# Kernel tuning notes

Hardware: AMD Instinct MI355X
Metric: run time of the kernel (lower is better)

## Reference

```python
import jax, jax.numpy as jnp
import numpy as np
import math

B, H, S, D = 2, 16, 2048, 128

def setup_inputs() -> dict:
    key = jax.random.key(0)
    kq, kk, kv = jax.random.split(key, 3)
    return {
        "query": jax.random.normal(kq, (B, H, S, D), dtype=jnp.float32),
        "key": jax.random.normal(kk, (B, H, S, D), dtype=jnp.float32),
        "value": jax.random.normal(kv, (B, H, S, D), dtype=jnp.float32),
        "m": 0,  # falsy mask: original's masked_fill was non-in-place (no-op) anyway
    }

def reference(query, key, value, m):
    d = query.shape[-1]
    # scores: [B, H, S, S]
    scores = jnp.einsum("bhqd,bhkd->bhqk", query, key) / math.sqrt(d)
    # NOTE: original torch code's masked_fill is not in-place, so the mask
    # never affects scores; we faithfully skip it (m is falsy here regardless).
    p_attn = jax.nn.softmax(scores, axis=-1)
    p_val = jnp.einsum("bhqk,bhkd->bhqd", p_attn, value)
    return (p_val, p_attn)
```

## Files before the change

### kernel.cpp

```cpp
#include <hip/hip_runtime.h>
#include <hip/hip_bf16.h>
#include <math.h>

#define S_LEN 2048
#define DHEAD 128
#define NH    32
#define BM    128
#define KT    32
#define NKT   (S_LEN / KT)
#define SCALE 0.08838834764831845f
#define CMAX  16.0f

typedef __attribute__((ext_vector_type(4))) float f32x4;
typedef __attribute__((ext_vector_type(8))) _Float16 f16x8;
typedef __attribute__((ext_vector_type(4))) unsigned short u16x4;
typedef __attribute__((ext_vector_type(8))) unsigned short u16x8;

static __device__ __forceinline__ f16x8 as_h8(u16x8 x) {
  return __builtin_bit_cast(f16x8, x);
}
static __device__ __forceinline__ unsigned short h16(float x) {
  _Float16 h = (_Float16)x;
  return __builtin_bit_cast(unsigned short, h);
}

#define BAR()                                                   \
  do {                                                          \
    __builtin_amdgcn_sched_barrier(0);                          \
    asm volatile("s_waitcnt lgkmcnt(0)" ::: "memory");          \
    __builtin_amdgcn_s_barrier();                               \
    __builtin_amdgcn_sched_barrier(0);                          \
  } while (0)

__global__ __launch_bounds__(512, 4) void attn_kernel(
    const float* __restrict__ Qg, const float* __restrict__ Kg,
    const float* __restrict__ Vg, float* __restrict__ out) {
  __shared__ __align__(16) unsigned short khf[2][KT * DHEAD];
  __shared__ __align__(16) unsigned short vtr[2][DHEAD * KT];

  const int tid = threadIdx.x;
  const int w  = tid >> 6;
  const int l  = tid & 63;
  const int lr = l & 15;
  const int lg = l >> 4;

  const int d_  = blockIdx.x;
  const int xcd = d_ & 7;
  const int slot = d_ >> 3;
  const int bh = xcd + 8 * (slot >> 4);
  const int qb = slot & 15;

  const size_t head_off = (size_t)bh * S_LEN * DHEAD;
  const float* Qh = Qg + head_off;
  const float* Kh = Kg + head_off;
  const float* Vh = Vg + head_off;
  float* Ov = out + head_off;
  float* Pa = out + (size_t)NH * S_LEN * DHEAD + (size_t)bh * S_LEN * S_LEN;

  const int ki0 = tid, ki1 = 512 + tid;
  const int kkv0 = ki0 >> 5, kd40 = ki0 & 31;
  const int kkv1 = ki1 >> 5, kd41 = ki1 & 31;
  const int vkv0 = (ki0 >> 2) & 31, vd40 = (ki0 & 3) | ((ki0 >> 7) << 2);
  const int vkv1 = (ki1 >> 2) & 31, vd41 = (ki1 & 3) | ((ki1 >> 7) << 2);

  float4 kxr0, kxr1, vx0, vx1;

  auto load_k = [&](int t) {
    const float4* s = (const float4*)(Kh + (size_t)t * KT * DHEAD);
    kxr0 = s[ki0];
    kxr1 = s[ki1];
  };
  auto load_v = [&](int t) {
    const float4* s = (const float4*)(Vh + (size_t)t * KT * DHEAD);
    vx0 = s[vkv0 * 32 + vd40];
    vx1 = s[vkv1 * 32 + vd41];
  };
  auto wk1 = [&](unsigned short* dst, int kv, int d4, float4 v) {
    u16x4 hv;
    hv[0] = h16(v.x); hv[1] = h16(v.y); hv[2] = h16(v.z); hv[3] = h16(v.w);
    *(u16x4*)&dst[kv * 128 + (((d4 >> 1) ^ (kv & 7)) << 3) + ((d4 & 1) << 2)] = hv;
  };
  auto write_k = [&](int b) {
    wk1(khf[b], kkv0, kd40, kxr0);
    wk1(khf[b], kkv1, kd41, kxr1);
  };
  auto wv1 = [&](unsigned short* dst, int kv, int d4, float4 v) {
    float f[4] = {v.x, v.y, v.z, v.w};
#pragma unroll
    for (int j = 0; j < 4; ++j) {
      int d = d4 * 4 + j;
      dst[d * 32 + (kv ^ (((d >> 1) & 3) << 3))] = h16(f[j]);
    }
  };
  auto write_v = [&](int b) {
    wv1(vtr[b], vkv0, vd40, vx0);
    wv1(vtr[b], vkv1, vd41, vx1);
  };
  auto ldk = [&](int b, int row, int kc) -> f16x8 {
    const unsigned short* base = khf[b] + row * 128;
    return as_h8(*(const u16x8*)&base[(((kc * 4 + lg) ^ (row & 7)) << 3)]);
  };

  load_k(0);
  const int qrow = qb * BM + w * 16 + lr;
  const float* qptr = Qh + (size_t)qrow * DHEAD;
  f16x8 qh[4];
#pragma unroll
  for (int kc = 0; kc < 4; ++kc) {
    const float4* qp4 = (const float4*)(qptr + kc * 32 + lg * 8);
    float4 a = qp4[0], b = qp4[1];
    float xs[8] = {a.x, a.y, a.z, a.w, b.x, b.y, b.z, b.w};
#pragma unroll
    for (int i = 0; i < 8; ++i) qh[kc][i] = (_Float16)(xs[i] * SCALE);
  }

  const f32x4 zero4 = {0.f, 0.f, 0.f, 0.f};

  float esum = 0.f;
  for (int t = 0; t < NKT; ++t) {
    const int b = t & 1;
    write_k(b);
    BAR();
    if (t + 1 < NKT) {
      load_k(t + 1);
    } else {
      load_k(0);
      load_v(0);
    }

    f32x4 sacc0 = zero4, sacc1 = zero4;
    __builtin_amdgcn_s_setprio(1);
#pragma unroll
    for (int kc = 0; kc < 4; ++kc) {
      f16x8 ka = ldk(b, lr, kc);
      f16x8 kb = ldk(b, lr + 16, kc);
      sacc0 = __builtin_amdgcn_mfma_f32_16x16x32_f16(ka, qh[kc], sacc0, 0, 0, 0);
      sacc1 = __builtin_amdgcn_mfma_f32_16x16x32_f16(kb, qh[kc], sacc1, 0, 0, 0);
    }
    __builtin_amdgcn_s_setprio(0);
#pragma unroll
    for (int r = 0; r < 4; ++r)
      esum += __expf(sacc0[r] - CMAX) + __expf(sacc1[r] - CMAX);
  }
  esum += __shfl_xor(esum, 16);
  esum += __shfl_xor(esum, 32);
  const float off_ = CMAX + logf(esum);

  f32x4 oacc[8];
#pragma unroll
  for (int dt = 0; dt < 8; ++dt) oacc[dt] = zero4;

  float* Prow = Pa + (size_t)(qb * BM + w * 16 + lr) * S_LEN;

  for (int t = 0; t < NKT; ++t) {
    const int b = t & 1;
    write_k(b);
    write_v(b);
    BAR();
    if (t + 1 < NKT) {
      load_k(t + 1);
      load_v(t + 1);
    }

    f32x4 sacc0 = zero4, sacc1 = zero4;
    __builtin_amdgcn_s_setprio(1);
#pragma unroll
    for (int kc = 0; kc < 4; ++kc) {
      f16x8 ka = ldk(b, lr, kc);
      f16x8 kb = ldk(b, lr + 16, kc);
      sacc0 = __builtin_amdgcn_mfma_f32_16x16x32_f16(ka, qh[kc], sacc0, 0, 0, 0);
      sacc1 = __builtin_amdgcn_mfma_f32_16x16x32_f16(kb, qh[kc], sacc1, 0, 0, 0);
    }
    __builtin_amdgcn_s_setprio(0);

    f32x4 pv0, pv1;
#pragma unroll
    for (int r = 0; r < 4; ++r) {
      pv0[r] = __expf(sacc0[r] - off_);
      pv1[r] = __expf(sacc1[r] - off_);
    }
    *(f32x4*)&Prow[t * KT + lg * 4] = pv0;
    *(f32x4*)&Prow[t * KT + 16 + lg * 4] = pv1;

    u16x8 pf;
    {
      unsigned pk[4];
#pragma unroll
      for (int r = 0; r < 4; ++r)
        pk[r] = __builtin_bit_cast(unsigned,
                  __builtin_amdgcn_cvt_pkrtz(pv0[r], pv1[r]));
      const int la = ((lg & 1) * 2) * 16 + lr;
      const int lb = la + 16;
      const bool hi = (lg & 2) != 0;
#pragma unroll
      for (int r = 0; r < 4; ++r) {
        unsigned ta = (unsigned)__shfl((int)pk[r], la, 64);
        unsigned tb = (unsigned)__shfl((int)pk[r], lb, 64);
        pf[r]     = (unsigned short)(hi ? (ta >> 16) : (ta & 0xffffu));
        pf[r + 4] = (unsigned short)(hi ? (tb >> 16) : (tb & 0xffffu));
      }
    }

    __builtin_amdgcn_s_setprio(1);
#pragma unroll
    for (int dt = 0; dt < 8; ++dt) {
      const int row = dt * 16 + lr;
      const unsigned short* vsrc = vtr[b];
      u16x8 vf = *(const u16x8*)&vsrc[row * 32 +
                                      ((lg * 8) ^ (((row >> 1) & 3) << 3))];
      oacc[dt] = __builtin_amdgcn_mfma_f32_16x16x32_f16(
          as_h8(pf), as_h8(vf), oacc[dt], 0, 0, 0);
    }
    __builtin_amdgcn_s_setprio(0);
  }

#pragma unroll
  for (int dt = 0; dt < 8; ++dt) {
#pragma unroll
    for (int r = 0; r < 4; ++r) {
      const int qloc = w * 16 + lg * 4 + r;
      Ov[(size_t)(qb * BM + qloc) * DHEAD + dt * 16 + lr] = oacc[dt][r];
    }
  }
}

extern "C" void kernel_launch(void* const* d_in, const int* in_sizes, int n_in,
                              void* d_out, int out_size, void* d_ws,
                              size_t ws_size, hipStream_t stream) {
  const float* Q = (const float*)d_in[0];
  const float* K = (const float*)d_in[1];
  const float* V = (const float*)d_in[2];
  float* out = (float*)d_out;
  (void)in_sizes; (void)n_in; (void)out_size; (void)d_ws; (void)ws_size;
  dim3 grid(NH * (S_LEN / BM));
  attn_kernel<<<grid, 512, 0, stream>>>(Q, K, V, out);
}
```

Before: 301.1 us.

## Shrink tiles to 64-row blocks with 16-key steps and 16x16x16 PV MFMA

Halves the query block to 64 rows and 256 threads, and halves the key tile to 16. The PV product now uses the 16x16x16 f16 MFMA directly on the score fragment, which removes the cross-lane shuffle repacking of probabilities. The V tile is stored transposed with a padded stride instead of an XOR swizzle. This trades less per-block K/V reuse and twice as many loop iterations and barriers for more blocks, simpler fragment handling and possibly better occupancy.

Result: slower. 438.2 us (+45.5%).

```diff
diff --git a/kernel.cpp b/kernel.cpp
--- a/kernel.cpp
+++ b/kernel.cpp
@@ -5,19 +5,24 @@
 #define S_LEN 2048
 #define DHEAD 128
 #define NH    32
-#define BM    128
-#define KT    32
+#define BM    64
+#define KT    16
 #define NKT   (S_LEN / KT)
+#define VPAD  20
 #define SCALE 0.08838834764831845f
 #define CMAX  16.0f
 
 typedef __attribute__((ext_vector_type(4))) float f32x4;
+typedef __attribute__((ext_vector_type(4))) _Float16 f16x4;
 typedef __attribute__((ext_vector_type(8))) _Float16 f16x8;
 typedef __attribute__((ext_vector_type(4))) unsigned short u16x4;
 typedef __attribute__((ext_vector_type(8))) unsigned short u16x8;
 
 static __device__ __forceinline__ f16x8 as_h8(u16x8 x) {
   return __builtin_bit_cast(f16x8, x);
+}
+static __device__ __forceinline__ f16x4 as_h4(u16x4 x) {
+  return __builtin_bit_cast(f16x4, x);
 }
 static __device__ __forceinline__ unsigned short h16(float x) {
   _Float16 h = (_Float16)x;
@@ -32,11 +37,11 @@
     __builtin_amdgcn_sched_barrier(0);                          \
   } while (0)
 
-__global__ __launch_bounds__(512, 4) void attn_kernel(
+__global__ __launch_bounds__(256) void attn_kernel(
     const float* __restrict__ Qg, const float* __restrict__ Kg,
     const float* __restrict__ Vg, float* __restrict__ out) {
   __shared__ __align__(16) unsigned short khf[2][KT * DHEAD];
-  __shared__ __align__(16) unsigned short vtr[2][DHEAD * KT];
+  __shared__ __align__(16) unsigned short vtr[2][DHEAD * VPAD];
 
   const int tid = threadIdx.x;
   const int w  = tid >> 6;
@@ -46,9 +51,9 @@
 
   const int d_  = blockIdx.x;
   const int xcd = d_ & 7;
-  const int slot = d_ >> 3;
-  const int bh = xcd + 8 * (slot >> 4);
-  const int qb = slot & 15;
+  const int idx = d_ >> 3;
+  const int bh = xcd + 8 * (idx >> 5);
+  const int qb = idx & 31;
 
   const size_t head_off = (size_t)bh * S_LEN * DHEAD;
   const float* Qh = Qg + head_off;
@@ -57,48 +62,45 @@
   float* Ov = out + head_off;
   float* Pa = out + (size_t)NH * S_LEN * DHEAD + (size_t)bh * S_LEN * S_LEN;
 
-  const int ki0 = tid, ki1 = 512 + tid;
-  const int kkv0 = ki0 >> 5, kd40 = ki0 & 31;
-  const int kkv1 = ki1 >> 5, kd41 = ki1 & 31;
-  const int vkv0 = (ki0 >> 2) & 31, vd40 = (ki0 & 3) | ((ki0 >> 7) << 2);
-  const int vkv1 = (ki1 >> 2) & 31, vd41 = (ki1 & 3) | ((ki1 >> 7) << 2);
-
-  float4 kxr0, kxr1, vx0, vx1;
-
+  const int kkv0 = tid >> 5, kd4 = tid & 31;
+  const int kkv1 = kkv0 + 8;
+  const int kaddr0 = kkv0 * 128 + (((kd4 >> 1) ^ (kkv0 & 7)) << 3) + ((kd4 & 1) << 2);
+  const int kaddr1 = kkv1 * 128 + (((kd4 >> 1) ^ (kkv1 & 7)) << 3) + ((kd4 & 1) << 2);
+  float4 kx0, kx1;
   auto load_k = [&](int t) {
     const float4* s = (const float4*)(Kh + (size_t)t * KT * DHEAD);
-    kxr0 = s[ki0];
-    kxr1 = s[ki1];
-  };
+    kx0 = s[tid];
+    kx1 = s[256 + tid];
+  };
+  auto write_k = [&](int b) {
+    u16x4 a, c;
+    a[0] = h16(kx0.x); a[1] = h16(kx0.y); a[2] = h16(kx0.z); a[3] = h16(kx0.w);
+    c[0] = h16(kx1.x); c[1] = h16(kx1.y); c[2] = h16(kx1.z); c[3] = h16(kx1.w);
+    *(u16x4*)&khf[b][kaddr0] = a;
+    *(u16x4*)&khf[b][kaddr1] = c;
+  };
+  auto ldk = [&](int b, int kc) -> f16x8 {
+    return as_h8(*(const u16x8*)&khf[b][lr * 128 + (((kc * 4 + lg) ^ (lr & 7)) << 3)]);
+  };
+
+  const int vkv = (tid >> 2) & 15;
+  const int vd40 = (tid & 3) | ((tid >> 6) << 2);
+  const int vd41 = vd40 + 16;
+  float4 vx0, vx1;
   auto load_v = [&](int t) {
     const float4* s = (const float4*)(Vh + (size_t)t * KT * DHEAD);
-    vx0 = s[vkv0 * 32 + vd40];
-    vx1 = s[vkv1 * 32 + vd41];
-  };
-  auto wk1 = [&](unsigned short* dst, int kv, int d4, float4 v) {
-    u16x4 hv;
-    hv[0] = h16(v.x); hv[1] = h16(v.y); hv[2] = h16(v.z); hv[3] = h16(v.w);
-    *(u16x4*)&dst[kv * 128 + (((d4 >> 1) ^ (kv & 7)) << 3) + ((d4 & 1) << 2)] = hv;
-  };
-  auto write_k = [&](int b) {
-    wk1(khf[b], kkv0, kd40, kxr0);
-    wk1(khf[b], kkv1, kd41, kxr1);
-  };
-  auto wv1 = [&](unsigned short* dst, int kv, int d4, float4 v) {
-    float f[4] = {v.x, v.y, v.z, v.w};
+    vx0 = s[vkv * 32 + vd40];
+    vx1 = s[vkv * 32 + vd41];
+  };
+  auto write_v = [&](int b) {
+    unsigned short* dst = vtr[b];
+    float f0[4] = {vx0.x, vx0.y, vx0.z, vx0.w};
+    float f1[4] = {vx1.x, vx1.y, vx1.z, vx1.w};
 #pragma unroll
     for (int j = 0; j < 4; ++j) {
-      int d = d4 * 4 + j;
-      dst[d * 32 + (kv ^ (((d >> 1) & 3) << 3))] = h16(f[j]);
-    }
-  };
-  auto write_v = [&](int b) {
-    wv1(vtr[b], vkv0, vd40, vx0);
-    wv1(vtr[b], vkv1, vd41, vx1);
-  };
-  auto ldk = [&](int b, int row, int kc) -> f16x8 {
-    const unsigned short* base = khf[b] + row * 128;
-    return as_h8(*(const u16x8*)&base[(((kc * 4 + lg) ^ (row & 7)) << 3)]);
+      dst[(vd40 * 4 + j) * VPAD + vkv] = h16(f0[j]);
+      dst[(vd41 * 4 + j) * VPAD + vkv] = h16(f1[j]);
+    }
   };
 
   load_k(0);
@@ -128,19 +130,15 @@
       load_v(0);
     }
 
-    f32x4 sacc0 = zero4, sacc1 = zero4;
+    f32x4 sacc = zero4;
     __builtin_amdgcn_s_setprio(1);
 #pragma unroll
-    for (int kc = 0; kc < 4; ++kc) {
-      f16x8 ka = ldk(b, lr, kc);
-      f16x8 kb = ldk(b, lr + 16, kc);
-      sacc0 = __builtin_amdgcn_mfma_f32_16x16x32_f16(ka, qh[kc], sacc0, 0, 0, 0);
-      sacc1 = __builtin_amdgcn_mfma_f32_16x16x32_f16(kb, qh[kc], sacc1, 0, 0, 0);
-    }
+    for (int kc = 0; kc < 4; ++kc)
+      sacc = __builtin_amdgcn_mfma_f32_16x16x32_f16(ldk(b, kc), qh[kc], sacc,
+                                                    0, 0, 0);
     __builtin_amdgcn_s_setprio(0);
 #pragma unroll
-    for (int r = 0; r < 4; ++r)
-      esum += __expf(sacc0[r] - CMAX) + __expf(sacc1[r] - CMAX);
+    for (int r = 0; r < 4; ++r) esum += __expf(sacc[r] - CMAX);
   }
   esum += __shfl_xor(esum, 16);
   esum += __shfl_xor(esum, 32);
@@ -162,54 +160,32 @@
       load_v(t + 1);
     }
 
-    f32x4 sacc0 = zero4, sacc1 = zero4;
+    f32x4 sacc = zero4;
     __builtin_amdgcn_s_setprio(1);
 #pragma unroll
-    for (int kc = 0; kc < 4; ++kc) {
-      f16x8 ka = ldk(b, lr, kc);
-      f16x8 kb = ldk(b, lr + 16, kc);
-      sacc0 = __builtin_amdgcn_mfma_f32_16x16x32_f16(ka, qh[kc], sacc0, 0, 0, 0);
-      sacc1 = __builtin_amdgcn_mfma_f32_16x16x32_f16(kb, qh[kc], sacc1, 0, 0, 0);
-    }
+    for (int kc = 0; kc < 4; ++kc)
+      sacc = __builtin_amdgcn_mfma_f32_16x16x32_f16(ldk(b, kc), qh[kc], sacc,
+                                                    0, 0, 0);
     __builtin_amdgcn_s_setprio(0);
 
-    f32x4 pv0, pv1;
-#pragma unroll
-    for (int r = 0; r < 4; ++r) {
-      pv0[r] = __expf(sacc0[r] - off_);
-      pv1[r] = __expf(sacc1[r] - off_);
-    }
-    *(f32x4*)&Prow[t * KT + lg * 4] = pv0;
-    *(f32x4*)&Prow[t * KT + 16 + lg * 4] = pv1;
-
-    u16x8 pf;
+    f32x4 pv;
+#pragma unroll
+    for (int r = 0; r < 4; ++r) pv[r] = __expf(sacc[r] - off_);
+    *(f32x4*)&Prow[t * KT + lg * 4] = pv;
+
+    f16x4 pa;
     {
-      unsigned pk[4];
-#pragma unroll
-      for (int r = 0; r < 4; ++r)
-        pk[r] = __builtin_bit_cast(unsigned,
-                  __builtin_amdgcn_cvt_pkrtz(pv0[r], pv1[r]));
-      const int la = ((lg & 1) * 2) * 16 + lr;
-      const int lb = la + 16;
-      const bool hi = (lg & 2) != 0;
-#pragma unroll
-      for (int r = 0; r < 4; ++r) {
-        unsigned ta = (unsigned)__shfl((int)pk[r], la, 64);
-        unsigned tb = (unsigned)__shfl((int)pk[r], lb, 64);
-        pf[r]     = (unsigned short)(hi ? (ta >> 16) : (ta & 0xffffu));
-        pf[r + 4] = (unsigned short)(hi ? (tb >> 16) : (tb & 0xffffu));
-      }
+      auto p01 = __builtin_amdgcn_cvt_pkrtz(pv[0], pv[1]);
+      auto p23 = __builtin_amdgcn_cvt_pkrtz(pv[2], pv[3]);
+      pa[0] = p01[0]; pa[1] = p01[1]; pa[2] = p23[0]; pa[3] = p23[1];
     }
 
     __builtin_amdgcn_s_setprio(1);
+    const unsigned short* vsrc = vtr[b];
 #pragma unroll
     for (int dt = 0; dt < 8; ++dt) {
-      const int row = dt * 16 + lr;
-      const unsigned short* vsrc = vtr[b];
-      u16x8 vf = *(const u16x8*)&vsrc[row * 32 +
-                                      ((lg * 8) ^ (((row >> 1) & 3) << 3))];
-      oacc[dt] = __builtin_amdgcn_mfma_f32_16x16x32_f16(
-          as_h8(pf), as_h8(vf), oacc[dt], 0, 0, 0);
+      f16x4 vb = as_h4(*(const u16x4*)&vsrc[(dt * 16 + lr) * VPAD + lg * 4]);
+      oacc[dt] = __builtin_amdgcn_mfma_f32_16x16x16f16(pa, vb, oacc[dt], 0, 0, 0);
     }
     __builtin_amdgcn_s_setprio(0);
   }
@@ -233,5 +209,5 @@
   float* out = (float*)d_out;
   (void)in_sizes; (void)n_in; (void)out_size; (void)d_ws; (void)ws_size;
   dim3 grid(NH * (S_LEN / BM));
-  attn_kernel<<<grid, 512, 0, stream>>>(Q, K, V, out);
-}
+  attn_kernel<<<grid, 256, 0, stream>>>(Q, K, V, out);
+}
```
